# Kernel tuning notes

Hardware: AMD Instinct MI355X
Metric: run time of the kernel (lower is better)

Reference implementation:

```python
import jax, jax.numpy as jnp
import numpy as np


def setup_inputs() -> dict:
    key = jax.random.key(0)
    ks = jax.random.split(key, 7)
    B, T, C = 8, 2048, 1024
    s = 0.02
    return {
        "x": jax.random.normal(ks[0], (B, T, C), dtype=jnp.float32),
        "Wq": jax.random.normal(ks[1], (C, C), dtype=jnp.float32) * s,
        "bq": jax.random.normal(ks[2], (C,), dtype=jnp.float32) * s,
        "Wk": jax.random.normal(ks[3], (C, C), dtype=jnp.float32) * s,
        "bk": jax.random.normal(ks[4], (C,), dtype=jnp.float32) * s,
        "Wv": jax.random.normal(ks[5], (C, C), dtype=jnp.float32) * s,
        "bv": jax.random.normal(ks[6], (C,), dtype=jnp.float32) * s,
    }


def reference(x, Wq, bq, Wk, bk, Wv, bv):
    # Single-head causal self-attention: Linear QKV -> QK^T/sqrt(C) -> causal mask -> softmax -> @V
    B, T, C = x.shape
    q = x @ Wq.T + bq  # [B,T,C]  (torch Linear: x @ W^T + b)
    k = x @ Wk.T + bk
    v = x @ Wv.T + bv
    scale = jnp.asarray(C, x.dtype) ** -0.5
    att = jnp.einsum("btc,bsc->bts", q, k) * scale  # [B,T,T]
    causal = jnp.tril(jnp.ones((T, T), dtype=bool))
    att = jnp.where(causal, att, jnp.finfo(att.dtype).min)
    att = jax.nn.softmax(att, axis=-1)
    out = jnp.einsum("bts,bsc->btc", att, v)  # [B,T,C]
    return out
```

## Files before the change

kernel.cpp:

```cpp
#include <hip/hip_runtime.h>
#include <hip/hip_bf16.h>

typedef __attribute__((ext_vector_type(8))) short bf16x8;
typedef __attribute__((ext_vector_type(4))) float floatx4;
typedef __attribute__((ext_vector_type(4))) short short4v;

__device__ inline short f2bf(float f) {
  union { float f; unsigned u; } v; v.f = f;
  unsigned r = v.u + 0x7fffu + ((v.u >> 16) & 1u);
  return (short)(r >> 16);
}

__device__ inline void gload_lds16(const short* g, short* l) {
  __builtin_amdgcn_global_load_lds(
      (const __attribute__((address_space(1))) unsigned int*)g,
      (__attribute__((address_space(3))) unsigned int*)l, 16, 0, 0);
}

__global__ __launch_bounds__(256) void cvt_kernel(
    const float* __restrict__ x, const float* __restrict__ wq,
    const float* __restrict__ wk, const float* __restrict__ wv,
    short* __restrict__ Xb, short* __restrict__ Wb) {
  long i4 = (long)(blockIdx.x * 256 + threadIdx.x) * 4;
  const float* src; short* dst; long off;
  if (i4 < 16777216L) {
    src = x; dst = Xb; off = i4;
  } else {
    long j = i4 - 16777216L;
    int mat = (int)(j >> 20);
    src = (mat == 0) ? wq : ((mat == 1) ? wk : wv);
    dst = Wb + ((long)mat << 20);
    off = j & 1048575L;
  }
  float4 v = *(const float4*)(src + off);
  short4v o; o.x = f2bf(v.x); o.y = f2bf(v.y); o.z = f2bf(v.z); o.w = f2bf(v.w);
  *(short4v*)(dst + off) = o;
}

__global__ __launch_bounds__(256) void qkv_gemm(
    const short* __restrict__ Xb, const short* __restrict__ Wb,
    const float* __restrict__ bq, const float* __restrict__ bk,
    const float* __restrict__ bv,
    short* __restrict__ Qf, short* __restrict__ Kf, short* __restrict__ Vf) {
  __shared__ short As[128 * 32];
  __shared__ short Bs[128 * 32];

  const int tid  = threadIdx.x;
  const int wave = tid >> 6, lane = tid & 63;
  const int quad = lane >> 4, l16 = lane & 15;
  const int wm = wave & 1, wn = wave >> 1;

  const int row0 = blockIdx.x * 128;
  const int col0 = blockIdx.y * 128;

  const int srow = wave * 16 + (lane >> 2);
  const int skof = (lane & 3) * 8;
  const short* gA0 = Xb + (size_t)(row0 + srow) * 1024 + skof;
  const short* gA1 = gA0 + (size_t)64 * 1024;
  const short* gB0 = Wb + (size_t)(col0 + srow) * 1024 + skof;
  const short* gB1 = gB0 + (size_t)64 * 1024;
  short* lA0 = As + (wave * 16) * 32 + lane * 8;
  short* lA1 = As + (64 + wave * 16) * 32 + lane * 8;
  short* lB0 = Bs + (wave * 16) * 32 + lane * 8;
  short* lB1 = Bs + (64 + wave * 16) * 32 + lane * 8;

  floatx4 acc[4][4] = {};

  for (int k = 0; k < 1024; k += 32) {
    gload_lds16(gA0 + k, lA0);
    gload_lds16(gA1 + k, lA1);
    gload_lds16(gB0 + k, lB0);
    gload_lds16(gB1 + k, lB1);
    __syncthreads();

    bf16x8 af[4], bfr[4];
#pragma unroll
    for (int mt = 0; mt < 4; mt++)
      af[mt] = *(const bf16x8*)(As + (wm * 64 + mt * 16 + l16) * 32 + quad * 8);
#pragma unroll
    for (int nb = 0; nb < 4; nb++)
      bfr[nb] = *(const bf16x8*)(Bs + (wn * 64 + nb * 16 + l16) * 32 + quad * 8);
#pragma unroll
    for (int mt = 0; mt < 4; mt++)
#pragma unroll
      for (int nb = 0; nb < 4; nb++)
        acc[mt][nb] = __builtin_amdgcn_mfma_f32_16x16x32_bf16(af[mt], bfr[nb], acc[mt][nb], 0, 0, 0);
    __syncthreads();
  }

#pragma unroll
  for (int nb = 0; nb < 4; nb++) {
    const int col = col0 + wn * 64 + nb * 16 + l16;
    const int mat = col >> 10;
    const int cn  = col & 1023;
    const float* bias = (mat == 0) ? bq : (mat == 1) ? bk : bv;
    const float bb = bias[cn];
    const float qs = (mat == 0) ? 0.03125f : 1.0f;
#pragma unroll
    for (int mt = 0; mt < 4; mt++) {
#pragma unroll
      for (int r = 0; r < 4; r++) {
        const int row = row0 + wm * 64 + mt * 16 + quad * 4 + r;
        short o = f2bf((acc[mt][nb][r] + bb) * qs);
        const int bat = row >> 11, t = row & 2047;
        if (mat <= 1) {
          const size_t idx = ((((size_t)bat * 128 + (t >> 4)) * 32 + (cn >> 5)) << 9)
                           + ((((cn >> 3) & 3) * 16 + (t & 15)) << 3) + (cn & 7);
          if (mat == 0) Qf[idx] = o; else Kf[idx] = o;
        } else {
          const size_t idx = ((((size_t)bat * 64 + (cn >> 4)) * 64 + (t >> 5)) << 9)
                           + ((((t >> 3) & 3) * 16 + (cn & 15)) << 3) + (t & 7);
          Vf[idx] = o;
        }
      }
    }
  }
}

__global__ __launch_bounds__(512, 2) void flash_attn(
    const short* __restrict__ Qf, const short* __restrict__ Kf,
    const short* __restrict__ Vf, float* __restrict__ out) {
  __shared__ float Sf[8][32][68];
  __shared__ short Pb[32][72];
  __shared__ float arow[32];
  __shared__ float lrow[32];

  const int b   = blockIdx.x & 7;
  const int p   = blockIdx.x >> 3;
  const int tid = threadIdx.x;
  const int wave = tid >> 6, lane = tid & 63;
  const int quad = lane >> 4, l16 = lane & 15;
  const int row = tid >> 4, sub = tid & 15;

#pragma unroll 1
  for (int pass = 0; pass < 2; ++pass) {
    const int j = pass ? p : (63 - p);
    const int ntiles = (j >> 1) + 1;
    const int gr = j * 32 + row;

    bf16x8 qfr[2][4];
#pragma unroll
    for (int mt = 0; mt < 2; mt++) {
      const short* qp = Qf + ((((size_t)b * 128 + j * 2 + mt) * 32 + wave * 4) << 9) + lane * 8;
#pragma unroll
      for (int dc = 0; dc < 4; dc++)
        qfr[mt][dc] = *(const bf16x8*)(qp + ((size_t)dc << 9));
    }

    floatx4 O[2][8] = {};
    float m_i = -1e30f, l_i = 0.0f;

    for (int kt = 0; kt < ntiles; kt++) {
      const short* kp = Kf + ((((size_t)b * 128 + kt * 4) * 32 + wave * 4) << 9) + lane * 8;
      bf16x8 kb[4][4];
#pragma unroll
      for (int nt = 0; nt < 4; nt++)
#pragma unroll
        for (int dc = 0; dc < 4; dc++)
          kb[nt][dc] = *(const bf16x8*)(kp + (((size_t)nt * 32 + dc) << 9));

      floatx4 s[2][4] = {};
#pragma unroll
      for (int nt = 0; nt < 4; nt++)
#pragma unroll
        for (int dc = 0; dc < 4; dc++)
#pragma unroll
          for (int mt = 0; mt < 2; mt++)
            s[mt][nt] = __builtin_amdgcn_mfma_f32_16x16x32_bf16(qfr[mt][dc], kb[nt][dc], s[mt][nt], 0, 0, 0);

#pragma unroll
      for (int mt = 0; mt < 2; mt++)
#pragma unroll
        for (int nt = 0; nt < 4; nt++)
#pragma unroll
          for (int r = 0; r < 4; r++)
            Sf[wave][mt * 16 + quad * 4 + r][nt * 16 + l16] = s[mt][nt][r];
      __syncthreads();

      const short* vp = Vf + ((((size_t)b * 64 + wave * 8) * 64 + kt * 2) << 9) + lane * 8;
      bf16x8 vb[2][8];
#pragma unroll
      for (int nb = 0; nb < 8; nb++)
#pragma unroll
        for (int kc = 0; kc < 2; kc++)
          vb[kc][nb] = *(const bf16x8*)(vp + (((size_t)nb * 64 + kc) << 9));

      const int kvbase = kt * 64;
      floatx4 vsum = {};
#pragma unroll
      for (int w = 0; w < 8; w++)
        vsum += *(const floatx4*)&Sf[w][row][sub * 4];
      float sv[4], mx = -1e30f;
#pragma unroll
      for (int jj = 0; jj < 4; jj++) {
        float v = vsum[jj];
        if (kvbase + sub * 4 + jj > gr) v = -1e30f;
        sv[jj] = v;
        mx = fmaxf(mx, v);
      }
#pragma unroll
      for (int msk = 1; msk <= 8; msk <<= 1)
        mx = fmaxf(mx, __shfl_xor(mx, msk, 64));
      const float mn = fmaxf(m_i, mx);
      const float alpha = __expf(m_i - mn);
      m_i = mn;
      float ps = 0.0f;
      short4v pb4;
#pragma unroll
      for (int jj = 0; jj < 4; jj++) {
        float pe = __expf(sv[jj] - mn);
        ps += pe;
        pb4[jj] = f2bf(pe);
      }
      *(short4v*)&Pb[row][sub * 4] = pb4;
#pragma unroll
      for (int msk = 1; msk <= 8; msk <<= 1)
        ps += __shfl_xor(ps, msk, 64);
      l_i = l_i * alpha + ps;
      if (sub == 0) arow[row] = alpha;
      __syncthreads();

      float al[2][4];
#pragma unroll
      for (int mt = 0; mt < 2; mt++)
#pragma unroll
        for (int r = 0; r < 4; r++) al[mt][r] = arow[mt * 16 + quad * 4 + r];
#pragma unroll
      for (int mt = 0; mt < 2; mt++)
#pragma unroll
        for (int nb = 0; nb < 8; nb++)
#pragma unroll
          for (int r = 0; r < 4; r++) O[mt][nb][r] *= al[mt][r];

#pragma unroll
      for (int kc = 0; kc < 2; kc++)
#pragma unroll
        for (int mt = 0; mt < 2; mt++) {
          bf16x8 pa = *(const bf16x8*)&Pb[mt * 16 + l16][kc * 32 + quad * 8];
#pragma unroll
          for (int nb = 0; nb < 8; nb++)
            O[mt][nb] = __builtin_amdgcn_mfma_f32_16x16x32_bf16(pa, vb[kc][nb], O[mt][nb], 0, 0, 0);
        }
    }

    if (sub == 0) lrow[row] = 1.0f / l_i;
    __syncthreads();
    float linv[2][4];
#pragma unroll
    for (int mt = 0; mt < 2; mt++)
#pragma unroll
      for (int r = 0; r < 4; r++) linv[mt][r] = lrow[mt * 16 + quad * 4 + r];
#pragma unroll
    for (int mt = 0; mt < 2; mt++)
#pragma unroll
      for (int nb = 0; nb < 8; nb++)
#pragma unroll
        for (int r = 0; r < 4; r++) {
          const int rr = j * 32 + mt * 16 + quad * 4 + r;
          const int cc = wave * 128 + nb * 16 + l16;
          out[((size_t)b * 2048 + rr) * 1024 + cc] = O[mt][nb][r] * linv[mt][r];
        }
  }
}

extern "C" void kernel_launch(void* const* d_in, const int* in_sizes, int n_in,
                              void* d_out, int out_size, void* d_ws, size_t ws_size,
                              hipStream_t stream) {
  const float* x  = (const float*)d_in[0];
  const float* Wq = (const float*)d_in[1];
  const float* bq = (const float*)d_in[2];
  const float* Wk = (const float*)d_in[3];
  const float* bk = (const float*)d_in[4];
  const float* Wv = (const float*)d_in[5];
  const float* bv = (const float*)d_in[6];
  float* out = (float*)d_out;

  char* ws = (char*)d_ws;
  short* Xb = (short*)(ws);
  short* Wb = (short*)(ws + 33554432);
  short* Qf = (short*)(ws + 39845888);
  short* Kf = (short*)(ws + 73400320);
  short* Vf = (short*)(ws + 106954752);

  cvt_kernel<<<19456, 256, 0, stream>>>(x, Wq, Wk, Wv, Xb, Wb);
  qkv_gemm<<<dim3(128, 24), 256, 0, stream>>>(Xb, Wb, bq, bk, bv, Qf, Kf, Vf);
  flash_attn<<<256, 512, 0, stream>>>(Qf, Kf, Vf, out);
}
```

Measured before the change: 436.4 us.

## Rewrite QKV GEMM with 256x256 tiles, 4-stage LDS pipeline and swizzle

The QKV projection GEMM moves from 128x128 tiles with a single LDS buffer to 256x256 tiles on 512 threads. It adds a 4-deep LDS ring of global-to-LDS loads, an XOR swizzle to avoid bank conflicts, and split MFMA phases with barriers and priority hints. Block IDs are remapped for L2 locality, and V stores are vectorised. The aim is to hide global-load latency and raise MFMA utilisation, at the cost of much more LDS and register pressure, which may limit occupancy.

New measurement: 386.1 us. 1.13x faster.

```diff
diff --git a/kernel.cpp b/kernel.cpp
--- a/kernel.cpp
+++ b/kernel.cpp
@@ -37,84 +37,141 @@
   *(short4v*)(dst + off) = o;
 }
 
-__global__ __launch_bounds__(256) void qkv_gemm(
+__global__ __launch_bounds__(512, 2) void qkv_gemm(
     const short* __restrict__ Xb, const short* __restrict__ Wb,
     const float* __restrict__ bq, const float* __restrict__ bk,
     const float* __restrict__ bv,
     short* __restrict__ Qf, short* __restrict__ Kf, short* __restrict__ Vf) {
-  __shared__ short As[128 * 32];
-  __shared__ short Bs[128 * 32];
+  __shared__ short As[4 * 8192];
+  __shared__ short Bs[4 * 8192];
 
   const int tid  = threadIdx.x;
   const int wave = tid >> 6, lane = tid & 63;
   const int quad = lane >> 4, l16 = lane & 15;
-  const int wm = wave & 1, wn = wave >> 1;
-
-  const int row0 = blockIdx.x * 128;
-  const int col0 = blockIdx.y * 128;
-
-  const int srow = wave * 16 + (lane >> 2);
-  const int skof = (lane & 3) * 8;
-  const short* gA0 = Xb + (size_t)(row0 + srow) * 1024 + skof;
-  const short* gA1 = gA0 + (size_t)64 * 1024;
-  const short* gB0 = Wb + (size_t)(col0 + srow) * 1024 + skof;
-  const short* gB1 = gB0 + (size_t)64 * 1024;
-  short* lA0 = As + (wave * 16) * 32 + lane * 8;
-  short* lA1 = As + (64 + wave * 16) * 32 + lane * 8;
-  short* lB0 = Bs + (wave * 16) * 32 + lane * 8;
-  short* lB1 = Bs + (64 + wave * 16) * 32 + lane * 8;
-
-  floatx4 acc[4][4] = {};
-
-  for (int k = 0; k < 1024; k += 32) {
-    gload_lds16(gA0 + k, lA0);
-    gload_lds16(gA1 + k, lA1);
-    gload_lds16(gB0 + k, lB0);
-    gload_lds16(gB1 + k, lB1);
-    __syncthreads();
-
-    bf16x8 af[4], bfr[4];
-#pragma unroll
-    for (int mt = 0; mt < 4; mt++)
-      af[mt] = *(const bf16x8*)(As + (wm * 64 + mt * 16 + l16) * 32 + quad * 8);
-#pragma unroll
-    for (int nb = 0; nb < 4; nb++)
-      bfr[nb] = *(const bf16x8*)(Bs + (wn * 64 + nb * 16 + l16) * 32 + quad * 8);
-#pragma unroll
-    for (int mt = 0; mt < 4; mt++)
-#pragma unroll
-      for (int nb = 0; nb < 4; nb++)
-        acc[mt][nb] = __builtin_amdgcn_mfma_f32_16x16x32_bf16(af[mt], bfr[nb], acc[mt][nb], 0, 0, 0);
-    __syncthreads();
-  }
-
-#pragma unroll
-  for (int nb = 0; nb < 4; nb++) {
-    const int col = col0 + wn * 64 + nb * 16 + l16;
-    const int mat = col >> 10;
-    const int cn  = col & 1023;
-    const float* bias = (mat == 0) ? bq : (mat == 1) ? bk : bv;
-    const float bb = bias[cn];
-    const float qs = (mat == 0) ? 0.03125f : 1.0f;
-#pragma unroll
-    for (int mt = 0; mt < 4; mt++) {
-#pragma unroll
-      for (int r = 0; r < 4; r++) {
-        const int row = row0 + wm * 64 + mt * 16 + quad * 4 + r;
-        short o = f2bf((acc[mt][nb][r] + bb) * qs);
-        const int bat = row >> 11, t = row & 2047;
-        if (mat <= 1) {
-          const size_t idx = ((((size_t)bat * 128 + (t >> 4)) * 32 + (cn >> 5)) << 9)
-                           + ((((cn >> 3) & 3) * 16 + (t & 15)) << 3) + (cn & 7);
-          if (mat == 0) Qf[idx] = o; else Kf[idx] = o;
-        } else {
-          const size_t idx = ((((size_t)bat * 64 + (cn >> 4)) * 64 + (t >> 5)) << 9)
-                           + ((((t >> 3) & 3) * 16 + (cn & 15)) << 3) + (t & 7);
-          Vf[idx] = o;
-        }
+  const int wm = wave >> 2, wn = wave & 3;
+
+  int bid = (int)blockIdx.x;
+  bid = (bid & 7) * 96 + (bid >> 3);
+  const int bx = bid / 12, by = bid % 12;
+  const int row0 = bx * 256, colbase = by * 256;
+
+  const int sr = tid >> 2;
+  const int sx = (((tid & 3) ^ ((tid >> 3) & 3)) << 3);
+  const short* gAbase = Xb + (size_t)(row0 + sr) * 1024 + sx;
+  const short* gBbase = Wb + (size_t)(colbase + sr) * 1024 + sx;
+  short* lA = (short*)As + tid * 8;
+  short* lB = (short*)Bs + tid * 8;
+
+#define STAGE_A(S) { const int _s = (S); const int _sl = (_s & 3) * 8192; \
+  gload_lds16(gAbase + (size_t)_s * 32, lA + _sl); \
+  gload_lds16(gAbase + (size_t)_s * 32 + 131072, lA + _sl + 4096); }
+#define STAGE_B(S) { const int _s = (S); const int _sl = (_s & 3) * 8192; \
+  gload_lds16(gBbase + (size_t)_s * 32, lB + _sl); \
+  gload_lds16(gBbase + (size_t)_s * 32 + 131072, lB + _sl + 4096); }
+
+  const int coff = (quad ^ ((l16 >> 1) & 3)) * 8;
+  const int aRow = (wm * 128 + l16) * 32 + coff;
+  const int bRow = (wn * 64 + l16) * 32 + coff;
+
+  floatx4 acc[8][4] = {};
+
+  STAGE_A(0) STAGE_B(0) STAGE_A(1) STAGE_B(1) STAGE_A(2) STAGE_B(2)
+  asm volatile("s_waitcnt vmcnt(4)" ::: "memory");
+  __builtin_amdgcn_s_barrier();
+
+#define PHASE_BAR() do { __builtin_amdgcn_sched_barrier(0); \
+                         __builtin_amdgcn_s_barrier(); } while (0)
+#define MFMA_ROW(MT, AF) \
+  acc[MT][0] = __builtin_amdgcn_mfma_f32_16x16x32_bf16(AF, bf0, acc[MT][0], 0, 0, 0); \
+  acc[MT][1] = __builtin_amdgcn_mfma_f32_16x16x32_bf16(AF, bf1, acc[MT][1], 0, 0, 0); \
+  acc[MT][2] = __builtin_amdgcn_mfma_f32_16x16x32_bf16(AF, bf2, acc[MT][2], 0, 0, 0); \
+  acc[MT][3] = __builtin_amdgcn_mfma_f32_16x16x32_bf16(AF, bf3, acc[MT][3], 0, 0, 0);
+
+#define STEP(S, WAIT) { \
+  const int sl_ = ((S) & 3) * 8192; \
+   \
+  bf16x8 af0 = *(const bf16x8*)(As + sl_ + aRow); \
+  bf16x8 af1 = *(const bf16x8*)(As + sl_ + aRow + 512); \
+  bf16x8 af2 = *(const bf16x8*)(As + sl_ + aRow + 1024); \
+  bf16x8 af3 = *(const bf16x8*)(As + sl_ + aRow + 1536); \
+  bf16x8 bf0 = *(const bf16x8*)(Bs + sl_ + bRow); \
+  bf16x8 bf1 = *(const bf16x8*)(Bs + sl_ + bRow + 512); \
+  bf16x8 bf2 = *(const bf16x8*)(Bs + sl_ + bRow + 1024); \
+  bf16x8 bf3 = *(const bf16x8*)(Bs + sl_ + bRow + 1536); \
+  STAGE_A(((S) + 3) & 31) \
+  PHASE_BAR(); \
+  __builtin_amdgcn_s_setprio(1); \
+  MFMA_ROW(0, af0) MFMA_ROW(1, af1) MFMA_ROW(2, af2) MFMA_ROW(3, af3) \
+  __builtin_amdgcn_s_setprio(0); \
+  PHASE_BAR(); \
+   \
+  bf16x8 ag0 = *(const bf16x8*)(As + sl_ + aRow + 2048); \
+  bf16x8 ag1 = *(const bf16x8*)(As + sl_ + aRow + 2560); \
+  bf16x8 ag2 = *(const bf16x8*)(As + sl_ + aRow + 3072); \
+  bf16x8 ag3 = *(const bf16x8*)(As + sl_ + aRow + 3584); \
+  STAGE_B(((S) + 3) & 31) \
+  PHASE_BAR(); \
+  __builtin_amdgcn_s_setprio(1); \
+  MFMA_ROW(4, ag0) MFMA_ROW(5, ag1) MFMA_ROW(6, ag2) MFMA_ROW(7, ag3) \
+  __builtin_amdgcn_s_setprio(0); \
+  if (WAIT) { asm volatile("s_waitcnt vmcnt(4)" ::: "memory"); } \
+  PHASE_BAR(); \
+}
+
+#pragma unroll 1
+  for (int kt = 0; kt < 16; ++kt) {
+    STEP(kt * 2, 0)
+    STEP(kt * 2 + 1, 1)
+  }
+
+  const int mat = by >> 2;
+  const float* bias = (mat == 0) ? bq : (mat == 1) ? bk : bv;
+  const float qs = (mat == 0) ? 0.03125f : 1.0f;
+  int cn[4]; float bb[4];
+#pragma unroll
+  for (int nb = 0; nb < 4; ++nb) {
+    cn[nb] = ((by & 3) << 8) + wn * 64 + nb * 16 + l16;
+    bb[nb] = bias[cn[nb]];
+  }
+
+  if (mat <= 1) {
+    short* dst = (mat == 0) ? Qf : Kf;
+#pragma unroll
+    for (int mt = 0; mt < 8; ++mt) {
+      const int rowb = row0 + wm * 128 + mt * 16 + quad * 4;
+      const int bat = rowb >> 11, t0 = rowb & 2047;
+#pragma unroll
+      for (int nb = 0; nb < 4; ++nb) {
+        const int c = cn[nb];
+        const size_t base = ((((size_t)bat * 128 + (t0 >> 4)) * 32 + (c >> 5)) << 9)
+                          + ((((c >> 3) & 3) * 16 + (t0 & 15)) << 3) + (c & 7);
+#pragma unroll
+        for (int r = 0; r < 4; ++r)
+          dst[base + (size_t)r * 8] = f2bf((acc[mt][nb][r] + bb[nb]) * qs);
       }
     }
-  }
+  } else {
+#pragma unroll
+    for (int mt = 0; mt < 8; ++mt) {
+      const int rowb = row0 + wm * 128 + mt * 16 + quad * 4;
+      const int bat = rowb >> 11, t0 = rowb & 2047;
+#pragma unroll
+      for (int nb = 0; nb < 4; ++nb) {
+        const int c = cn[nb];
+        const size_t base = ((((size_t)bat * 64 + (c >> 4)) * 64 + (t0 >> 5)) << 9)
+                          + ((((t0 >> 3) & 3) * 16 + (c & 15)) << 3) + (t0 & 7);
+        short4v ov;
+#pragma unroll
+        for (int r = 0; r < 4; ++r) ov[r] = f2bf(acc[mt][nb][r] + bb[nb]);
+        *(short4v*)(Vf + base) = ov;
+      }
+    }
+  }
+#undef STEP
+#undef MFMA_ROW
+#undef PHASE_BAR
+#undef STAGE_A
+#undef STAGE_B
 }
 
 __global__ __launch_bounds__(512, 2) void flash_attn(
@@ -283,6 +340,6 @@
   short* Vf = (short*)(ws + 106954752);
 
   cvt_kernel<<<19456, 256, 0, stream>>>(x, Wq, Wk, Wv, Xb, Wb);
-  qkv_gemm<<<dim3(128, 24), 256, 0, stream>>>(Xb, Wb, bq, bk, bv, Qf, Kf, Vf);
+  qkv_gemm<<<dim3(768), 512, 0, stream>>>(Xb, Wb, bq, bk, bv, Qf, Kf, Vf);
   flash_attn<<<256, 512, 0, stream>>>(Qf, Kf, Vf, out);
 }
```
